# Kernel optimization log

Hardware: AMD Instinct MI355X
Metric: run time of the kernel (lower is better)

Reference implementation:

```python
import jax, jax.numpy as jnp
import numpy as np

N = 512          # number of proposals
C = 1024         # in_channels
FLAT = C * 7 * 7 # 50176, fc1 input dim
D = 1024         # hidden / feat_dim / attention dim
SCALE = 1.0 / np.sqrt(float(D))


def setup_inputs() -> dict:
    key = jax.random.key(0)
    ks = jax.random.split(key, 20)
    w = lambda k, shape: (jax.random.normal(k, shape, jnp.float32) * 0.01)
    inp = {"x": jax.random.normal(ks[0], (N, C, 7, 7), jnp.float32)}
    # SelsaHead fc layers
    inp["fc1_w"] = w(ks[1], (D, FLAT)); inp["fc1_b"] = jnp.zeros((D,), jnp.float32)
    inp["fc2_w"] = w(ks[2], (D, D));    inp["fc2_b"] = jnp.zeros((D,), jnp.float32)
    # attention_1 (semantic_aggregation): fc1, fc2, 1x1 conv (stored as [D,D] matrix)
    inp["a1_fc1_w"] = w(ks[3], (D, D)); inp["a1_fc1_b"] = jnp.zeros((D,), jnp.float32)
    inp["a1_fc2_w"] = w(ks[4], (D, D)); inp["a1_fc2_b"] = jnp.zeros((D,), jnp.float32)
    inp["a1_conv_w"] = w(ks[5], (D, D)); inp["a1_conv_b"] = jnp.zeros((D,), jnp.float32)
    # attention_2
    inp["a2_fc1_w"] = w(ks[6], (D, D)); inp["a2_fc1_b"] = jnp.zeros((D,), jnp.float32)
    inp["a2_fc2_w"] = w(ks[7], (D, D)); inp["a2_fc2_b"] = jnp.zeros((D,), jnp.float32)
    inp["a2_conv_w"] = w(ks[8], (D, D)); inp["a2_conv_b"] = jnp.zeros((D,), jnp.float32)
    return inp


def _semantic_aggregation(x, w1, b1, w2, b2, cw, cb):
    # x: [N, D]. Single-head dense attention over proposals, values = x itself.
    q = x @ w1.T + b1                      # [N, D]
    k = x @ w2.T + b2                      # [N, D]
    p = jax.nn.softmax((q @ k.T) * SCALE, axis=-1)  # [N, N]
    out = p @ x                            # [N, D]  (values are raw x)
    return out @ cw.T + cb                 # 1x1 conv == linear [N, D]


def reference(x, fc1_w, fc1_b, fc2_w, fc2_b,
              a1_fc1_w, a1_fc1_b, a1_fc2_w, a1_fc2_b, a1_conv_w, a1_conv_b,
              a2_fc1_w, a2_fc1_b, a2_fc2_w, a2_fc2_b, a2_conv_w, a2_conv_b):
    out = x.reshape(x.shape[0], -1) @ fc1_w.T + fc1_b        # [N, D]
    r1 = _semantic_aggregation(out, a1_fc1_w, a1_fc1_b, a1_fc2_w, a1_fc2_b,
                               a1_conv_w, a1_conv_b)
    h = jax.nn.relu(out + r1)
    h = h @ fc2_w.T + fc2_b                                  # [N, D]
    r2 = _semantic_aggregation(h, a2_fc1_w, a2_fc1_b, a2_fc2_w, a2_fc2_b,
                               a2_conv_w, a2_conv_b)
    return jax.nn.relu(h + r2 + out)                         # [N, D]
```

## Files before the change

### kernel.cpp

```cpp
#include <hip/hip_runtime.h>
#include <hip/hip_bf16.h>

typedef __attribute__((ext_vector_type(8))) short short8;
typedef __attribute__((ext_vector_type(4))) float f32x4;

#define N_PROP 512
#define DHID   1024
#define KFLAT  50176
#define SM_SCALE 0.03125f

__device__ inline short f2bf(float x) {
  __hip_bfloat16 b = __float2bfloat16(x);
  return __builtin_bit_cast(short, b);
}
__device__ inline float bf2f(unsigned short u) {
  unsigned int x = (unsigned int)u << 16;
  return __builtin_bit_cast(float, x);
}

__device__ inline void pinned_bar() {
  asm volatile("s_waitcnt lgkmcnt(0)" ::: "memory");
  __builtin_amdgcn_s_barrier();
  asm volatile("" ::: "memory");
}

__global__ __launch_bounds__(1024, 4)
void gemm_fc1(const float* __restrict__ A, const float* __restrict__ B,
              __hip_bfloat16* __restrict__ parts)
{
  constexpr int BK = 32;
  constexpr int KLEN = 1568, NT = KLEN / BK;
  __shared__ short sA[2][256 * 32];
  __shared__ short sB[2][256 * 32];

  const int n = gridDim.x;
  int lid = blockIdx.x;
  lid = (lid & 7) * (n >> 3) + (lid >> 3);
  const int y    = lid >> 3;
  const int tile = lid & 7;
  const int tm = tile >> 2;
  const int tn = tile & 3;

  const int k0 = y * KLEN;

  const int tid  = threadIdx.x;
  const int lane = tid & 63;
  const int wid  = tid >> 6;
  const int wr = wid >> 2, wc = wid & 3;
  const int l16 = lane & 15, kq = lane >> 4;

  const float* Ab = A + (size_t)(tm * 256) * KFLAT;
  const float* Bb = B + (size_t)(tn * 256) * KFLAT;

  const int srow = tid >> 2;
  const int sc   = tid & 3;
  const int sphys = sc ^ ((srow >> 1) & 3);

  f32x4 acc[4][4];
  #pragma unroll
  for (int i = 0; i < 4; ++i)
    #pragma unroll
    for (int j = 0; j < 4; ++j)
      acc[i][j] = (f32x4){0.f, 0.f, 0.f, 0.f};

  float4 ra0, ra1, rb0, rb1;

  auto loadAB = [&](int kk) {
    const float* pa = Ab + (size_t)srow * KFLAT + kk + sc * 8;
    const float* pb = Bb + (size_t)srow * KFLAT + kk + sc * 8;
    ra0 = *(const float4*)pa; ra1 = *(const float4*)(pa + 4);
    rb0 = *(const float4*)pb; rb1 = *(const float4*)(pb + 4);
  };
  auto storeAB = [&](int b) {
    short8 s;
    s[0]=f2bf(ra0.x); s[1]=f2bf(ra0.y); s[2]=f2bf(ra0.z); s[3]=f2bf(ra0.w);
    s[4]=f2bf(ra1.x); s[5]=f2bf(ra1.y); s[6]=f2bf(ra1.z); s[7]=f2bf(ra1.w);
    *(short8*)&sA[b][srow * 32 + sphys * 8] = s;
    s[0]=f2bf(rb0.x); s[1]=f2bf(rb0.y); s[2]=f2bf(rb0.z); s[3]=f2bf(rb0.w);
    s[4]=f2bf(rb1.x); s[5]=f2bf(rb1.y); s[6]=f2bf(rb1.z); s[7]=f2bf(rb1.w);
    *(short8*)&sB[b][srow * 32 + sphys * 8] = s;
  };
  auto compute = [&](int b) {
    short8 af[4], bf[4];
    #pragma unroll
    for (int i = 0; i < 4; ++i) {
      int R  = wr * 64 + i * 16 + l16;
      int ph = kq ^ ((R >> 1) & 3);
      af[i] = *(short8*)&sA[b][R * 32 + ph * 8];
    }
    #pragma unroll
    for (int j = 0; j < 4; ++j) {
      int R  = wc * 64 + j * 16 + l16;
      int ph = kq ^ ((R >> 1) & 3);
      bf[j] = *(short8*)&sB[b][R * 32 + ph * 8];
    }
    #pragma unroll
    for (int i = 0; i < 4; ++i)
      #pragma unroll
      for (int j = 0; j < 4; ++j)
        acc[i][j] = __builtin_amdgcn_mfma_f32_16x16x32_bf16(af[i], bf[j], acc[i][j], 0, 0, 0);
  };

  loadAB(k0);
  storeAB(0);
  loadAB(k0 + BK);
  pinned_bar();

  int cur = 0;
  for (int t = 0; t < NT; ++t) {
    if (t + 1 < NT) {
      storeAB(cur ^ 1);
      if (t + 2 < NT) loadAB(k0 + (t + 2) * BK);
    }
    compute(cur);
    pinned_bar();
    cur ^= 1;
  }

  __hip_bfloat16* P = parts + (size_t)y * (N_PROP * DHID);
  const int crow0 = tm * 256 + wr * 64;
  const int ccol0 = tn * 256 + wc * 64;
  #pragma unroll
  for (int i = 0; i < 4; ++i)
    #pragma unroll
    for (int j = 0; j < 4; ++j)
      #pragma unroll
      for (int e = 0; e < 4; ++e) {
        int r = crow0 + i * 16 + kq * 4 + e;
        int c = ccol0 + j * 16 + l16;
        P[(size_t)r * DHID + c] = __float2bfloat16(acc[i][j][e]);
      }
}

template<int BM, int BN, int BK, int MINW>
__global__ __launch_bounds__(256, MINW)
void gemm_nt(const float* __restrict__ A, int lda,
             const float* __restrict__ B1, const float* __restrict__ B2, int ldb,
             float* __restrict__ C, __hip_bfloat16* __restrict__ Cb, int ldc,
             int tiles_per_slice, int tiles_n,
             int klen, int ktot,
             size_t c_split_stride, size_t c_z_stride,
             const float* __restrict__ bias1, const float* __restrict__ bias2,
             const float* __restrict__ res1, const float* __restrict__ res2,
             float* __restrict__ Ct, int ldct,
             int do_relu)
{
  constexpr int BKP = BK + 8;
  constexpr int WM = BM / 2, WN = BN / 2;
  constexpr int FM = WM / 16, FN = WN / 16;
  constexpr int NCH = BK / 8;
  constexpr int CHA = (BM * BK) / (8 * 256);
  constexpr int CHB = (BN * BK) / (8 * 256);

  __shared__ short As[BM * BKP];
  __shared__ short Bs[BN * BKP];

  const int n = gridDim.x;
  int lid = blockIdx.x;
  lid = (lid & 7) * (n >> 3) + (lid >> 3);

  const int y    = lid / tiles_per_slice;
  const int tile = lid % tiles_per_slice;
  const int tm = tile / tiles_n;
  const int tn = tile % tiles_n;

  const int k0 = y * klen;
  const int krem = ktot - k0;
  const int klen_eff = krem < klen ? krem : klen;
  const int nt = klen_eff / BK;

  const size_t coff = (size_t)y * c_split_stride + (size_t)blockIdx.z * c_z_stride;
  if (C)  C  += coff;
  if (Cb) Cb += coff;
  const float* B    = blockIdx.z ? B2 : B1;
  const float* bias = blockIdx.z ? bias2 : bias1;

  const int tid  = threadIdx.x;
  const int lane = tid & 63;
  const int wid  = tid >> 6;
  const int wm = wid >> 1, wn = wid & 1;
  const int l16 = lane & 15, kq = lane >> 4;

  const float* Abase = A + (size_t)(tm * BM) * lda;
  const float* Bbase = B + (size_t)(tn * BN) * ldb;

  f32x4 acc[FM][FN];
  #pragma unroll
  for (int i = 0; i < FM; ++i)
    #pragma unroll
    for (int j = 0; j < FN; ++j)
      acc[i][j] = (f32x4){0.f, 0.f, 0.f, 0.f};

  float4 ra[CHA][2], rb[CHB][2];

  auto loadA = [&](int kk) {
    #pragma unroll
    for (int i = 0; i < CHA; ++i) {
      int ch = tid + i * 256;
      int r = ch / NCH, cc = ch % NCH;
      const float* p = Abase + (size_t)r * lda + kk + cc * 8;
      ra[i][0] = *(const float4*)p;
      ra[i][1] = *(const float4*)(p + 4);
    }
  };
  auto loadB = [&](int kk) {
    #pragma unroll
    for (int i = 0; i < CHB; ++i) {
      int ch = tid + i * 256;
      int r = ch / NCH, cc = ch % NCH;
      const float* p = Bbase + (size_t)r * ldb + kk + cc * 8;
      rb[i][0] = *(const float4*)p;
      rb[i][1] = *(const float4*)(p + 4);
    }
  };
  auto storeAB = [&]() {
    #pragma unroll
    for (int i = 0; i < CHA; ++i) {
      int ch = tid + i * 256;
      int r = ch / NCH, cc = ch % NCH;
      float4 u = ra[i][0], v = ra[i][1];
      short8 s;
      s[0]=f2bf(u.x); s[1]=f2bf(u.y); s[2]=f2bf(u.z); s[3]=f2bf(u.w);
      s[4]=f2bf(v.x); s[5]=f2bf(v.y); s[6]=f2bf(v.z); s[7]=f2bf(v.w);
      *(short8*)&As[r * BKP + cc * 8] = s;
    }
    #pragma unroll
    for (int i = 0; i < CHB; ++i) {
      int ch = tid + i * 256;
      int r = ch / NCH, cc = ch % NCH;
      float4 u = rb[i][0], v = rb[i][1];
      short8 s;
      s[0]=f2bf(u.x); s[1]=f2bf(u.y); s[2]=f2bf(u.z); s[3]=f2bf(u.w);
      s[4]=f2bf(v.x); s[5]=f2bf(v.y); s[6]=f2bf(v.z); s[7]=f2bf(v.w);
      *(short8*)&Bs[r * BKP + cc * 8] = s;
    }
  };

  loadA(k0); loadB(k0);
  storeAB();
  pinned_bar();

  for (int t = 0; t < nt; ++t) {
    if (t + 1 < nt) { loadA(k0 + (t + 1) * BK); loadB(k0 + (t + 1) * BK); }

    #pragma unroll
    for (int ks = 0; ks < BK / 32; ++ks) {
      short8 af[FM], bf[FN];
      #pragma unroll
      for (int i = 0; i < FM; ++i)
        af[i] = *(short8*)&As[(wm * WM + i * 16 + l16) * BKP + ks * 32 + kq * 8];
      #pragma unroll
      for (int j = 0; j < FN; ++j)
        bf[j] = *(short8*)&Bs[(wn * WN + j * 16 + l16) * BKP + ks * 32 + kq * 8];
      #pragma unroll
      for (int i = 0; i < FM; ++i)
        #pragma unroll
        for (int j = 0; j < FN; ++j)
          acc[i][j] = __builtin_amdgcn_mfma_f32_16x16x32_bf16(af[i], bf[j], acc[i][j], 0, 0, 0);
    }

    pinned_bar();
    if (t + 1 < nt) storeAB();
    pinned_bar();
  }

  const int crow0 = tm * BM + wm * WM;
  const int ccol0 = tn * BN + wn * WN;
  #pragma unroll
  for (int i = 0; i < FM; ++i)
    #pragma unroll
    for (int j = 0; j < FN; ++j)
      #pragma unroll
      for (int e = 0; e < 4; ++e) {
        int r = crow0 + i * 16 + kq * 4 + e;
        int c = ccol0 + j * 16 + l16;
        float v = acc[i][j][e];
        if (bias) v += bias[c];
        if (res1) v += res1[(size_t)r * ldc + c];
        if (res2) v += res2[(size_t)r * ldc + c];
        if (do_relu) v = fmaxf(v, 0.f);
        if (Cb) Cb[(size_t)r * ldc + c] = __float2bfloat16(v);
        else    C [(size_t)r * ldc + c] = v;
        if (Ct) Ct[(size_t)c * ldct + r] = v;
      }
}

__global__ __launch_bounds__(256)
void reduce_bias(const __hip_bfloat16* __restrict__ parts, int sk, size_t stride,
                 const float* __restrict__ bias, float* __restrict__ out)
{
  int idx4 = blockIdx.x * 256 + threadIdx.x;
  int c4 = idx4 & (DHID / 4 - 1);
  float4 b = *(const float4*)(bias + (size_t)c4 * 4);
  float s0 = b.x, s1 = b.y, s2 = b.z, s3 = b.w;
  for (int i = 0; i < sk; ++i) {
    const __hip_bfloat16* p = parts + (size_t)i * stride + (size_t)idx4 * 4;
    ushort4 u = *(const ushort4*)p;
    s0 += bf2f(u.x); s1 += bf2f(u.y); s2 += bf2f(u.z); s3 += bf2f(u.w);
  }
  float4 o = {s0, s1, s2, s3};
  *(float4*)(out + (size_t)idx4 * 4) = o;
}

__global__ __launch_bounds__(256)
void transpose_k(const float* __restrict__ in, float* __restrict__ out, int R, int Cc)
{
  __shared__ float t[32][33];
  int bx = blockIdx.x * 32;
  int by = blockIdx.y * 32;
  int tx = threadIdx.x & 31, ty = threadIdx.x >> 5;
  #pragma unroll
  for (int i = 0; i < 4; ++i)
    t[ty + i * 8][tx] = in[(size_t)(by + ty + i * 8) * Cc + bx + tx];
  __syncthreads();
  #pragma unroll
  for (int i = 0; i < 4; ++i)
    out[(size_t)(bx + ty + i * 8) * R + by + tx] = t[tx][ty + i * 8];
}

__global__ __launch_bounds__(256)
void softmax_rows(float* __restrict__ x, float scale)
{
  int row = blockIdx.x;
  float* p = x + (size_t)row * N_PROP;
  int tid = threadIdx.x;
  float a = p[tid] * scale;
  float b = p[tid + 256] * scale;
  float m = fmaxf(a, b);
  #pragma unroll
  for (int o = 32; o > 0; o >>= 1) m = fmaxf(m, __shfl_xor(m, o));
  __shared__ float sm[4], ss[4];
  int w = tid >> 6;
  if ((tid & 63) == 0) sm[w] = m;
  __syncthreads();
  m = fmaxf(fmaxf(sm[0], sm[1]), fmaxf(sm[2], sm[3]));
  float ea = __expf(a - m), eb = __expf(b - m);
  float s = ea + eb;
  #pragma unroll
  for (int o = 32; o > 0; o >>= 1) s += __shfl_xor(s, o);
  if ((tid & 63) == 0) ss[w] = s;
  __syncthreads();
  s = ss[0] + ss[1] + ss[2] + ss[3];
  float inv = 1.f / s;
  p[tid] = ea * inv;
  p[tid + 256] = eb * inv;
}

extern "C" void kernel_launch(void* const* d_in, const int* in_sizes, int n_in,
                              void* d_out, int out_size, void* d_ws, size_t ws_size,
                              hipStream_t stream)
{
  (void)in_sizes; (void)n_in; (void)out_size; (void)ws_size;
  const float* x      = (const float*)d_in[0];
  const float* fc1_w  = (const float*)d_in[1];
  const float* fc1_b  = (const float*)d_in[2];
  const float* fc2_w  = (const float*)d_in[3];
  const float* fc2_b  = (const float*)d_in[4];
  const float* a1w1   = (const float*)d_in[5];
  const float* a1b1   = (const float*)d_in[6];
  const float* a1w2   = (const float*)d_in[7];
  const float* a1b2   = (const float*)d_in[8];
  const float* a1cw   = (const float*)d_in[9];
  const float* a1cb   = (const float*)d_in[10];
  const float* a2w1   = (const float*)d_in[11];
  const float* a2b1   = (const float*)d_in[12];
  const float* a2w2   = (const float*)d_in[13];
  const float* a2b2   = (const float*)d_in[14];
  const float* a2cw   = (const float*)d_in[15];
  const float* a2cb   = (const float*)d_in[16];
  float* out = (float*)d_out;

  char* ws = (char*)d_ws;
  const size_t SZ = (size_t)N_PROP * DHID * 4;
  float* out0   = (float*)(ws + 0 * SZ);
  float* h0     = (float*)(ws + 1 * SZ);
  float* h1     = (float*)(ws + 2 * SZ);
  float* T      = (float*)(ws + 3 * SZ);
  float* q      = (float*)(ws + 4 * SZ);
  float* k      = (float*)(ws + 5 * SZ);
  float* att    = (float*)(ws + 6 * SZ);
  float* logits = (float*)(ws + 7 * SZ);
  __hip_bfloat16* parts =
      (__hip_bfloat16*)(ws + 7 * SZ + (size_t)N_PROP * N_PROP * 4);

  const size_t ND = (size_t)N_PROP * DHID;
  const int SK = 32;
  dim3 blk(256);

  gemm_fc1<<<dim3(8 * SK), dim3(1024), 0, stream>>>(x, fc1_w, parts);
  reduce_bias<<<(N_PROP * DHID) / 1024, blk, 0, stream>>>(parts, SK, ND, fc1_b, out0);

  transpose_k<<<dim3(DHID / 32, N_PROP / 32), blk, 0, stream>>>(out0, T, N_PROP, DHID);
  gemm_nt<32, 64, 128, 2><<<dim3(256, 1, 2), blk, 0, stream>>>(
      out0, DHID, a1w1, a1w2, DHID,
      q, nullptr, DHID,
      256, 16, DHID, DHID,
      0, ND,
      a1b1, a1b2, nullptr, nullptr, nullptr, 0, 0);
  gemm_nt<32, 32, 128, 2><<<dim3(256), blk, 0, stream>>>(
      q, DHID, k, nullptr, DHID,
      logits, nullptr, N_PROP,
      256, 16, DHID, DHID,
      0, 0,
      nullptr, nullptr, nullptr, nullptr, nullptr, 0, 0);
  softmax_rows<<<N_PROP, blk, 0, stream>>>(logits, SM_SCALE);
  gemm_nt<32, 64, 128, 2><<<dim3(256), blk, 0, stream>>>(
      logits, N_PROP, T, nullptr, N_PROP,
      att, nullptr, DHID,
      256, 16, N_PROP, N_PROP,
      0, 0,
      nullptr, nullptr, nullptr, nullptr, nullptr, 0, 0);
  gemm_nt<32, 64, 128, 2><<<dim3(256), blk, 0, stream>>>(
      att, DHID, a1cw, nullptr, DHID,
      h0, nullptr, DHID,
      256, 16, DHID, DHID,
      0, 0,
      a1cb, nullptr, out0, nullptr, nullptr, 0, 1);
  gemm_nt<32, 64, 128, 2><<<dim3(256), blk, 0, stream>>>(
      h0, DHID, fc2_w, nullptr, DHID,
      h1, nullptr, DHID,
      256, 16, DHID, DHID,
      0, 0,
      fc2_b, nullptr, nullptr, nullptr, T, N_PROP, 0);

  gemm_nt<32, 64, 128, 2><<<dim3(256, 1, 2), blk, 0, stream>>>(
      h1, DHID, a2w1, a2w2, DHID,
      q, nullptr, DHID,
      256, 16, DHID, DHID,
      0, ND,
      a2b1, a2b2, nullptr, nullptr, nullptr, 0, 0);
  gemm_nt<32, 32, 128, 2><<<dim3(256), blk, 0, stream>>>(
      q, DHID, k, nullptr, DHID,
      logits, nullptr, N_PROP,
      256, 16, DHID, DHID,
      0, 0,
      nullptr, nullptr, nullptr, nullptr, nullptr, 0, 0);
  softmax_rows<<<N_PROP, blk, 0, stream>>>(logits, SM_SCALE);
  gemm_nt<32, 64, 128, 2><<<dim3(256), blk, 0, stream>>>(
      logits, N_PROP, T, nullptr, N_PROP,
      att, nullptr, DHID,
      256, 16, N_PROP, N_PROP,
      0, 0,
      nullptr, nullptr, nullptr, nullptr, nullptr, 0, 0);
  gemm_nt<32, 64, 128, 2><<<dim3(256), blk, 0, stream>>>(
      att, DHID, a2cw, nullptr, DHID,
      out, nullptr, DHID,
      256, 16, DHID, DHID,
      0, 0,
      a2cb, nullptr, h1, out0, nullptr, 0, 1);
}
```

Measured before the change: 221.1 us.

## Keep intermediates in bf16, double-buffer LDS in GEMMs, fuse reduce with transpose

Intermediate activations (out0, q, k, att, h0, h1, transposed copies and the softmax probabilities) are now stored as bf16, so the downstream GEMMs load A and B operands without an fp32-to-bf16 conversion and read half the bytes. The generic GEMM gains a two-stage LDS double buffer with register prefetch two tiles ahead, which drops one barrier per K step. The split-K reduction is fused with the transpose into a single kernel. The second attention now uses a separate bf16 transpose of h1 produced in the fc2 epilogue. The cost is more LDS per block and register pressure from the prefetch buffers.

```diff
diff --git a/kernel.cpp b/kernel.cpp
--- a/kernel.cpp
+++ b/kernel.cpp
@@ -12,10 +12,6 @@
 __device__ inline short f2bf(float x) {
   __hip_bfloat16 b = __float2bfloat16(x);
   return __builtin_bit_cast(short, b);
-}
-__device__ inline float bf2f(unsigned short u) {
-  unsigned int x = (unsigned int)u << 16;
-  return __builtin_bit_cast(float, x);
 }
 
 __device__ inline void pinned_bar() {
@@ -132,47 +128,37 @@
       }
 }
 
-template<int BM, int BN, int BK, int MINW>
-__global__ __launch_bounds__(256, MINW)
-void gemm_nt(const float* __restrict__ A, int lda,
-             const float* __restrict__ B1, const float* __restrict__ B2, int ldb,
+template<int BM, int BN, int BK, typename BT>
+__global__ __launch_bounds__(256, 2)
+void gemm_bf(const __hip_bfloat16* __restrict__ A, int lda,
+             const BT* __restrict__ B1, const BT* __restrict__ B2, int ldb,
              float* __restrict__ C, __hip_bfloat16* __restrict__ Cb, int ldc,
-             int tiles_per_slice, int tiles_n,
-             int klen, int ktot,
-             size_t c_split_stride, size_t c_z_stride,
+             int tiles_n, int ktot, size_t c_z_stride,
              const float* __restrict__ bias1, const float* __restrict__ bias2,
              const float* __restrict__ res1, const float* __restrict__ res2,
-             float* __restrict__ Ct, int ldct,
-             int do_relu)
+             __hip_bfloat16* __restrict__ Ct, int ldct, int do_relu)
 {
   constexpr int BKP = BK + 8;
   constexpr int WM = BM / 2, WN = BN / 2;
   constexpr int FM = WM / 16, FN = WN / 16;
-  constexpr int NCH = BK / 8;
-  constexpr int CHA = (BM * BK) / (8 * 256);
-  constexpr int CHB = (BN * BK) / (8 * 256);
-
-  __shared__ short As[BM * BKP];
-  __shared__ short Bs[BN * BKP];
+  constexpr int NC = BK / 8;
+  constexpr int NA = (BM * BK) / (8 * 256);
+  constexpr int NB = (BN * BK) / (8 * 256);
+  constexpr bool BF = sizeof(BT) == 2;
+
+  __shared__ short As[2][BM * BKP];
+  __shared__ short Bs[2][BN * BKP];
 
   const int n = gridDim.x;
   int lid = blockIdx.x;
   lid = (lid & 7) * (n >> 3) + (lid >> 3);
-
-  const int y    = lid / tiles_per_slice;
-  const int tile = lid % tiles_per_slice;
-  const int tm = tile / tiles_n;
-  const int tn = tile % tiles_n;
-
-  const int k0 = y * klen;
-  const int krem = ktot - k0;
-  const int klen_eff = krem < klen ? krem : klen;
-  const int nt = klen_eff / BK;
-
-  const size_t coff = (size_t)y * c_split_stride + (size_t)blockIdx.z * c_z_stride;
-  if (C)  C  += coff;
-  if (Cb) Cb += coff;
-  const float* B    = blockIdx.z ? B2 : B1;
+  const int tm = lid / tiles_n;
+  const int tn = lid % tiles_n;
+  const int nt = ktot / BK;
+
+  if (C)  C  += (size_t)blockIdx.z * c_z_stride;
+  if (Cb) Cb += (size_t)blockIdx.z * c_z_stride;
+  const BT* B      = blockIdx.z ? B2 : B1;
   const float* bias = blockIdx.z ? bias2 : bias1;
 
   const int tid  = threadIdx.x;
@@ -181,8 +167,8 @@
   const int wm = wid >> 1, wn = wid & 1;
   const int l16 = lane & 15, kq = lane >> 4;
 
-  const float* Abase = A + (size_t)(tm * BM) * lda;
-  const float* Bbase = B + (size_t)(tn * BN) * ldb;
+  const __hip_bfloat16* Ab = A + (size_t)(tm * BM) * lda;
+  const BT*             Bb = B + (size_t)(tn * BN) * ldb;
 
   f32x4 acc[FM][FN];
   #pragma unroll
@@ -191,77 +177,82 @@
     for (int j = 0; j < FN; ++j)
       acc[i][j] = (f32x4){0.f, 0.f, 0.f, 0.f};
 
-  float4 ra[CHA][2], rb[CHB][2];
-
-  auto loadA = [&](int kk) {
-    #pragma unroll
-    for (int i = 0; i < CHA; ++i) {
+  short8 rah[2][NA];
+  short8 rbh[2][NB];
+  float4 rbf[2][NB][2];
+
+  auto loadAB = [&](int kk, int s) {
+    #pragma unroll
+    for (int i = 0; i < NA; ++i) {
       int ch = tid + i * 256;
-      int r = ch / NCH, cc = ch % NCH;
-      const float* p = Abase + (size_t)r * lda + kk + cc * 8;
-      ra[i][0] = *(const float4*)p;
-      ra[i][1] = *(const float4*)(p + 4);
-    }
-  };
-  auto loadB = [&](int kk) {
-    #pragma unroll
-    for (int i = 0; i < CHB; ++i) {
+      int r = ch / NC, c = (ch % NC) * 8;
+      rah[s][i] = *(const short8*)(Ab + (size_t)r * lda + kk + c);
+    }
+    #pragma unroll
+    for (int i = 0; i < NB; ++i) {
       int ch = tid + i * 256;
-      int r = ch / NCH, cc = ch % NCH;
-      const float* p = Bbase + (size_t)r * ldb + kk + cc * 8;
-      rb[i][0] = *(const float4*)p;
-      rb[i][1] = *(const float4*)(p + 4);
-    }
-  };
-  auto storeAB = [&]() {
-    #pragma unroll
-    for (int i = 0; i < CHA; ++i) {
+      int r = ch / NC, c = (ch % NC) * 8;
+      if constexpr (BF) {
+        rbh[s][i] = *(const short8*)(Bb + (size_t)r * ldb + kk + c);
+      } else {
+        const float* p = (const float*)Bb + (size_t)r * ldb + kk + c;
+        rbf[s][i][0] = *(const float4*)p;
+        rbf[s][i][1] = *(const float4*)(p + 4);
+      }
+    }
+  };
+  auto storeAB = [&](int s, int b) {
+    #pragma unroll
+    for (int i = 0; i < NA; ++i) {
       int ch = tid + i * 256;
-      int r = ch / NCH, cc = ch % NCH;
-      float4 u = ra[i][0], v = ra[i][1];
-      short8 s;
-      s[0]=f2bf(u.x); s[1]=f2bf(u.y); s[2]=f2bf(u.z); s[3]=f2bf(u.w);
-      s[4]=f2bf(v.x); s[5]=f2bf(v.y); s[6]=f2bf(v.z); s[7]=f2bf(v.w);
-      *(short8*)&As[r * BKP + cc * 8] = s;
-    }
-    #pragma unroll
-    for (int i = 0; i < CHB; ++i) {
+      int r = ch / NC, c = (ch % NC) * 8;
+      *(short8*)&As[b][r * BKP + c] = rah[s][i];
+    }
+    #pragma unroll
+    for (int i = 0; i < NB; ++i) {
       int ch = tid + i * 256;
-      int r = ch / NCH, cc = ch % NCH;
-      float4 u = rb[i][0], v = rb[i][1];
-      short8 s;
-      s[0]=f2bf(u.x); s[1]=f2bf(u.y); s[2]=f2bf(u.z); s[3]=f2bf(u.w);
-      s[4]=f2bf(v.x); s[5]=f2bf(v.y); s[6]=f2bf(v.z); s[7]=f2bf(v.w);
-      *(short8*)&Bs[r * BKP + cc * 8] = s;
-    }
-  };
-
-  loadA(k0); loadB(k0);
-  storeAB();
-  pinned_bar();
-
-  for (int t = 0; t < nt; ++t) {
-    if (t + 1 < nt) { loadA(k0 + (t + 1) * BK); loadB(k0 + (t + 1) * BK); }
-
+      int r = ch / NC, c = (ch % NC) * 8;
+      if constexpr (BF) {
+        *(short8*)&Bs[b][r * BKP + c] = rbh[s][i];
+      } else {
+        float4 u = rbf[s][i][0], v = rbf[s][i][1];
+        short8 w;
+        w[0]=f2bf(u.x); w[1]=f2bf(u.y); w[2]=f2bf(u.z); w[3]=f2bf(u.w);
+        w[4]=f2bf(v.x); w[5]=f2bf(v.y); w[6]=f2bf(v.z); w[7]=f2bf(v.w);
+        *(short8*)&Bs[b][r * BKP + c] = w;
+      }
+    }
+  };
+  auto compute = [&](int b) {
     #pragma unroll
     for (int ks = 0; ks < BK / 32; ++ks) {
       short8 af[FM], bf[FN];
       #pragma unroll
       for (int i = 0; i < FM; ++i)
-        af[i] = *(short8*)&As[(wm * WM + i * 16 + l16) * BKP + ks * 32 + kq * 8];
+        af[i] = *(short8*)&As[b][(wm * WM + i * 16 + l16) * BKP + ks * 32 + kq * 8];
       #pragma unroll
       for (int j = 0; j < FN; ++j)
-        bf[j] = *(short8*)&Bs[(wn * WN + j * 16 + l16) * BKP + ks * 32 + kq * 8];
+        bf[j] = *(short8*)&Bs[b][(wn * WN + j * 16 + l16) * BKP + ks * 32 + kq * 8];
       #pragma unroll
       for (int i = 0; i < FM; ++i)
         #pragma unroll
         for (int j = 0; j < FN; ++j)
           acc[i][j] = __builtin_amdgcn_mfma_f32_16x16x32_bf16(af[i], bf[j], acc[i][j], 0, 0, 0);
     }
-
+  };
+
+  loadAB(0, 0);
+  storeAB(0, 0);
+  loadAB(BK, 1);
+  pinned_bar();
+
+  int cur = 0;
+  for (int t = 0; t < nt; ++t) {
+    if (t + 1 < nt) storeAB((t + 1) & 1, cur ^ 1);
+    if (t + 2 < nt) loadAB((t + 2) * BK, t & 1);
+    compute(cur);
     pinned_bar();
-    if (t + 1 < nt) storeAB();
-    pinned_bar();
+    cur ^= 1;
   }
 
   const int crow0 = tm * BM + wm * WM;
@@ -279,53 +270,46 @@
         if (res1) v += res1[(size_t)r * ldc + c];
         if (res2) v += res2[(size_t)r * ldc + c];
         if (do_relu) v = fmaxf(v, 0.f);
+        if (C)  C [(size_t)r * ldc + c] = v;
         if (Cb) Cb[(size_t)r * ldc + c] = __float2bfloat16(v);
-        else    C [(size_t)r * ldc + c] = v;
-        if (Ct) Ct[(size_t)c * ldct + r] = v;
+        if (Ct) Ct[(size_t)c * ldct + r] = __float2bfloat16(v);
       }
 }
 
 __global__ __launch_bounds__(256)
-void reduce_bias(const __hip_bfloat16* __restrict__ parts, int sk, size_t stride,
-                 const float* __restrict__ bias, float* __restrict__ out)
+void reduce_t(const __hip_bfloat16* __restrict__ parts, const float* __restrict__ bias,
+              float* __restrict__ out0f, __hip_bfloat16* __restrict__ out0b,
+              __hip_bfloat16* __restrict__ T)
 {
-  int idx4 = blockIdx.x * 256 + threadIdx.x;
-  int c4 = idx4 & (DHID / 4 - 1);
-  float4 b = *(const float4*)(bias + (size_t)c4 * 4);
-  float s0 = b.x, s1 = b.y, s2 = b.z, s3 = b.w;
-  for (int i = 0; i < sk; ++i) {
-    const __hip_bfloat16* p = parts + (size_t)i * stride + (size_t)idx4 * 4;
-    ushort4 u = *(const ushort4*)p;
-    s0 += bf2f(u.x); s1 += bf2f(u.y); s2 += bf2f(u.z); s3 += bf2f(u.w);
-  }
-  float4 o = {s0, s1, s2, s3};
-  *(float4*)(out + (size_t)idx4 * 4) = o;
-}
-
-__global__ __launch_bounds__(256)
-void transpose_k(const float* __restrict__ in, float* __restrict__ out, int R, int Cc)
-{
-  __shared__ float t[32][33];
+  __shared__ float tile[32][33];
   int bx = blockIdx.x * 32;
   int by = blockIdx.y * 32;
   int tx = threadIdx.x & 31, ty = threadIdx.x >> 5;
   #pragma unroll
+  for (int i = 0; i < 4; ++i) {
+    int r = by + ty + i * 8, c = bx + tx;
+    float s = bias[c];
+    for (int sl = 0; sl < 32; ++sl)
+      s += __bfloat162float(parts[(size_t)sl * (N_PROP * DHID) + (size_t)r * DHID + c]);
+    out0f[(size_t)r * DHID + c] = s;
+    out0b[(size_t)r * DHID + c] = __float2bfloat16(s);
+    tile[ty + i * 8][tx] = s;
+  }
+  __syncthreads();
+  #pragma unroll
   for (int i = 0; i < 4; ++i)
-    t[ty + i * 8][tx] = in[(size_t)(by + ty + i * 8) * Cc + bx + tx];
-  __syncthreads();
-  #pragma unroll
-  for (int i = 0; i < 4; ++i)
-    out[(size_t)(bx + ty + i * 8) * R + by + tx] = t[tx][ty + i * 8];
+    T[(size_t)(bx + ty + i * 8) * N_PROP + by + tx] =
+        __float2bfloat16(tile[tx][ty + i * 8]);
 }
 
 __global__ __launch_bounds__(256)
-void softmax_rows(float* __restrict__ x, float scale)
+void softmax_rows(const float* __restrict__ x, __hip_bfloat16* __restrict__ p, float scale)
 {
   int row = blockIdx.x;
-  float* p = x + (size_t)row * N_PROP;
+  const float* q = x + (size_t)row * N_PROP;
   int tid = threadIdx.x;
-  float a = p[tid] * scale;
-  float b = p[tid + 256] * scale;
+  float a = q[tid] * scale;
+  float b = q[tid + 256] * scale;
   float m = fmaxf(a, b);
   #pragma unroll
   for (int o = 32; o > 0; o >>= 1) m = fmaxf(m, __shfl_xor(m, o));
@@ -342,8 +326,8 @@
   __syncthreads();
   s = ss[0] + ss[1] + ss[2] + ss[3];
   float inv = 1.f / s;
-  p[tid] = ea * inv;
-  p[tid + 256] = eb * inv;
+  p[(size_t)row * N_PROP + tid]       = __float2bfloat16(ea * inv);
+  p[(size_t)row * N_PROP + tid + 256] = __float2bfloat16(eb * inv);
 }
 
 extern "C" void kernel_launch(void* const* d_in, const int* in_sizes, int n_in,
@@ -370,82 +354,66 @@
   const float* a2cb   = (const float*)d_in[16];
   float* out = (float*)d_out;
 
+  typedef __hip_bfloat16 bf16;
   char* ws = (char*)d_ws;
-  const size_t SZ = (size_t)N_PROP * DHID * 4;
-  float* out0   = (float*)(ws + 0 * SZ);
-  float* h0     = (float*)(ws + 1 * SZ);
-  float* h1     = (float*)(ws + 2 * SZ);
-  float* T      = (float*)(ws + 3 * SZ);
-  float* q      = (float*)(ws + 4 * SZ);
-  float* k      = (float*)(ws + 5 * SZ);
-  float* att    = (float*)(ws + 6 * SZ);
-  float* logits = (float*)(ws + 7 * SZ);
-  __hip_bfloat16* parts =
-      (__hip_bfloat16*)(ws + 7 * SZ + (size_t)N_PROP * N_PROP * 4);
-
+  const size_t MB = 1024 * 1024;
+  float* out0f  = (float*)(ws + 0 * MB);
+  float* h1f    = (float*)(ws + 2 * MB);
+  float* logits = (float*)(ws + 4 * MB);
+  bf16*  out0b  = (bf16*)(ws + 5 * MB);
+  bf16*  T      = (bf16*)(ws + 6 * MB);
+  bf16*  q      = (bf16*)(ws + 7 * MB);
+  bf16*  k      = (bf16*)(ws + 8 * MB);
+  bf16*  att    = (bf16*)(ws + 9 * MB);
+  bf16*  h0b    = (bf16*)(ws + 10 * MB);
+  bf16*  h1b    = (bf16*)(ws + 11 * MB);
+  bf16*  T2     = (bf16*)(ws + 12 * MB);
+  bf16*  pb     = (bf16*)(ws + 13 * MB);
+  bf16*  parts  = (bf16*)(ws + 14 * MB);
   const size_t ND = (size_t)N_PROP * DHID;
-  const int SK = 32;
   dim3 blk(256);
 
-  gemm_fc1<<<dim3(8 * SK), dim3(1024), 0, stream>>>(x, fc1_w, parts);
-  reduce_bias<<<(N_PROP * DHID) / 1024, blk, 0, stream>>>(parts, SK, ND, fc1_b, out0);
-
-  transpose_k<<<dim3(DHID / 32, N_PROP / 32), blk, 0, stream>>>(out0, T, N_PROP, DHID);
-  gemm_nt<32, 64, 128, 2><<<dim3(256, 1, 2), blk, 0, stream>>>(
-      out0, DHID, a1w1, a1w2, DHID,
-      q, nullptr, DHID,
-      256, 16, DHID, DHID,
-      0, ND,
+  gemm_fc1<<<dim3(256), dim3(1024), 0, stream>>>(x, fc1_w, parts);
+  reduce_t<<<dim3(DHID / 32, N_PROP / 32), blk, 0, stream>>>(
+      parts, fc1_b, out0f, out0b, T);
+
+  gemm_bf<32, 64, 128, float><<<dim3(256, 1, 2), blk, 0, stream>>>(
+      out0b, DHID, a1w1, a1w2, DHID,
+      nullptr, q, DHID, 16, DHID, ND,
       a1b1, a1b2, nullptr, nullptr, nullptr, 0, 0);
-  gemm_nt<32, 32, 128, 2><<<dim3(256), blk, 0, stream>>>(
+  gemm_bf<32, 32, 128, bf16><<<dim3(256), blk, 0, stream>>>(
       q, DHID, k, nullptr, DHID,
-      logits, nullptr, N_PROP,
-      256, 16, DHID, DHID,
-      0, 0,
+      logits, nullptr, N_PROP, 16, DHID, 0,
       nullptr, nullptr, nullptr, nullptr, nullptr, 0, 0);
-  softmax_rows<<<N_PROP, blk, 0, stream>>>(logits, SM_SCALE);
-  gemm_nt<32, 64, 128, 2><<<dim3(256), blk, 0, stream>>>(
-      logits, N_PROP, T, nullptr, N_PROP,
-      att, nullptr, DHID,
-      256, 16, N_PROP, N_PROP,
-      0, 0,
+  softmax_rows<<<N_PROP, blk, 0, stream>>>(logits, pb, SM_SCALE);
+  gemm_bf<32, 64, 128, bf16><<<dim3(256), blk, 0, stream>>>(
+      pb, N_PROP, T, nullptr, N_PROP,
+      nullptr, att, DHID, 16, N_PROP, 0,
       nullptr, nullptr, nullptr, nullptr, nullptr, 0, 0);
-  gemm_nt<32, 64, 128, 2><<<dim3(256), blk, 0, stream>>>(
+  gemm_bf<32, 64, 128, float><<<dim3(256), blk, 0, stream>>>(
       att, DHID, a1cw, nullptr, DHID,
-      h0, nullptr, DHID,
-      256, 16, DHID, DHID,
-      0, 0,
-      a1cb, nullptr, out0, nullptr, nullptr, 0, 1);
-  gemm_nt<32, 64, 128, 2><<<dim3(256), blk, 0, stream>>>(
-      h0, DHID, fc2_w, nullptr, DHID,
-      h1, nullptr, DHID,
-      256, 16, DHID, DHID,
-      0, 0,
-      fc2_b, nullptr, nullptr, nullptr, T, N_PROP, 0);
-
-  gemm_nt<32, 64, 128, 2><<<dim3(256, 1, 2), blk, 0, stream>>>(
-      h1, DHID, a2w1, a2w2, DHID,
-      q, nullptr, DHID,
-      256, 16, DHID, DHID,
-      0, ND,
+      nullptr, h0b, DHID, 16, DHID, 0,
+      a1cb, nullptr, out0f, nullptr, nullptr, 0, 1);
+  gemm_bf<32, 64, 128, float><<<dim3(256), blk, 0, stream>>>(
+      h0b, DHID, fc2_w, nullptr, DHID,
+      h1f, h1b, DHID, 16, DHID, 0,
+      fc2_b, nullptr, nullptr, nullptr, T2, N_PROP, 0);
+
+  gemm_bf<32, 64, 128, float><<<dim3(256, 1, 2), blk, 0, stream>>>(
+      h1b, DHID, a2w1, a2w2, DHID,
+      nullptr, q, DHID, 16, DHID, ND,
       a2b1, a2b2, nullptr, nullptr, nullptr, 0, 0);
-  gemm_nt<32, 32, 128, 2><<<dim3(256), blk, 0, stream>>>(
+  gemm_bf<32, 32, 128, bf16><<<dim3(256), blk, 0, stream>>>(
       q, DHID, k, nullptr, DHID,
-      logits, nullptr, N_PROP,
-      256, 16, DHID, DHID,
-      0, 0,
+      logits, nullptr, N_PROP, 16, DHID, 0,
       nullptr, nullptr, nullptr, nullptr, nullptr, 0, 0);
-  softmax_rows<<<N_PROP, blk, 0, stream>>>(logits, SM_SCALE);
-  gemm_nt<32, 64, 128, 2><<<dim3(256), blk, 0, stream>>>(
-      logits, N_PROP, T, nullptr, N_PROP,
-      att, nullptr, DHID,
-      256, 16, N_PROP, N_PROP,
-      0, 0,
+  softmax_rows<<<N_PROP, blk, 0, stream>>>(logits, pb, SM_SCALE);
+  gemm_bf<32, 64, 128, bf16><<<dim3(256), blk, 0, stream>>>(
+      pb, N_PROP, T2, nullptr, N_PROP,
+      nullptr, att, DHID, 16, N_PROP, 0,
       nullptr, nullptr, nullptr, nullptr, nullptr, 0, 0);
-  gemm_nt<32, 64, 128, 2><<<dim3(256), blk, 0, stream>>>(
+  gemm_bf<32, 64, 128, float><<<dim3(256), blk, 0, stream>>>(
       att, DHID, a2cw, nullptr, DHID,
-      out, nullptr, DHID,
-      256, 16, DHID, DHID,
-      0, 0,
-      a2cb, nullptr, h1, out0, nullptr, 0, 1);
-}
+      out, nullptr, DHID, 16, DHID, 0,
+      a2cb, nullptr, h1f, out0f, nullptr, 0, 1);
+}
```

Result: slower. 818.5 us (+270.2%).
